# Kernel tuning notes

Measured on AMD Instinct MI355X. Metric: run time of the kernel, lower is better.

The kernel has to match this reference:

```python
import jax, jax.numpy as jnp
import numpy as np

C0 = 32          # cs[0] == cs[1] with planes=[32,32,...], cr=1.0
CIN = 4
EPS = 1e-5

# ---------- host-side coordinate hashing (mirrors F.sphash / F.sphashquery) ----------

def _enc(c):
    # unique int64 code per (x,y,z); +2 shift keeps offset-adjusted coords positive
    return (c[:, 0] + 2).astype(np.int64) + (c[:, 1] + 2).astype(np.int64) * 1024 \
        + (c[:, 2] + 2).astype(np.int64) * 1024 * 1024

def _lookup(sorted_codes, q):
    pos = np.searchsorted(sorted_codes, q)
    pos = np.minimum(pos, len(sorted_codes) - 1)
    return np.where(sorted_codes[pos] == q, pos, -1).astype(np.int32)

def _offsets(r):
    return np.array([[i, j, k] for i in r for j in r for k in r], np.int64)


def setup_inputs() -> dict:
    rng = np.random.default_rng(0)
    N0 = 400000
    pts = rng.integers(0, [400, 400, 40], size=(600000, 3)).astype(np.int64)
    codes = _enc(pts)
    codes_u, idx = np.unique(codes, return_index=True)
    assert len(codes_u) >= N0
    coords0, codes0 = pts[idx][:N0], codes_u[:N0]   # sorted by hash code

    off27, off8 = _offsets([-1, 0, 1]), _offsets([0, 1])
    # ks=3 stride=1 kernel map at level 0: nbr0[k, i] = index of coords0[i]+off27[k] (or -1)
    nbr0 = np.stack([_lookup(codes0, _enc(coords0 + o)) for o in off27])

    # stride-2 downsample coords (level 1)
    c1all = coords0 // 2
    codes1_u, i1 = np.unique(_enc(c1all), return_index=True)
    coords1 = c1all[i1]
    # ks=2 stride=2 kernel map: output voxel gathers inputs at 2*out + {0,1}^3
    down1 = np.stack([_lookup(codes0, _enc(coords1 * 2 + o)) for o in off8])
    # ks=3 stride=1 kernel map at level 1
    nbr1 = np.stack([_lookup(codes1_u, _enc(coords1 + o)) for o in off27])

    key = jax.random.key(0)
    ks = jax.random.split(key, 10)

    def w(k, K, ci, co):
        return jax.random.normal(k, (K, ci, co), jnp.float32) * (1.0 / np.sqrt(K * ci))

    return {
        "voxel_features": jax.random.normal(ks[0], (N0, CIN), jnp.float32),
        "W_stem1": w(ks[1], 27, CIN, C0),
        "W_stem2": w(ks[2], 27, C0, C0),
        "W_down":  w(ks[3], 8,  C0, C0),
        "W_r1a":   w(ks[4], 27, C0, C0),
        "W_r1b":   w(ks[5], 27, C0, C0),
        "W_r2a":   w(ks[6], 27, C0, C0),
        "W_r2b":   w(ks[7], 27, C0, C0),
        "gammas": jnp.ones((7, C0), jnp.float32),
        "betas":  jnp.zeros((7, C0), jnp.float32),
        "nbr0":  jnp.asarray(nbr0),
        "down1": jnp.asarray(down1),
        "nbr1":  jnp.asarray(nbr1),
    }


# ---------- sparse conv: gather-GEMM-scatter per kernel offset ----------

def _spconv(feat, nbr, W):
    # feat [N, Ci], nbr [K, M] (-1 = no neighbor), W [K, Ci, Co] -> out [M, Co]
    def step(acc, kw):
        idx, Wk = kw
        g = jnp.where((idx >= 0)[:, None], feat[jnp.maximum(idx, 0)], 0.0)
        return acc + g @ Wk, None
    acc0 = jnp.zeros((nbr.shape[1], W.shape[-1]), feat.dtype)
    out, _ = jax.lax.scan(step, acc0, (nbr, W))
    return out


def _bn(x, g, b):
    # BatchNorm1d, training-mode statistics (biased var), gamma/beta affine
    mu = x.mean(0)
    var = x.var(0)
    return (x - mu) * jax.lax.rsqrt(var + EPS) * g + b


def _cbr(x, nbr, W, g, b):
    return jax.nn.relu(_bn(_spconv(x, nbr, W), g, b))


def reference(voxel_features, W_stem1, W_stem2, W_down, W_r1a, W_r1b, W_r2a, W_r2b,
              gammas, betas, nbr0, down1, nbr1):
    g, b = gammas, betas
    # stem: two ks=3 sparse convs + BN + ReLU at level 0
    x = _cbr(voxel_features, nbr0, W_stem1, g[0], b[0])
    x = _cbr(x, nbr0, W_stem2, g[1], b[1])
    # stage1: BasicConvolutionBlock (ks=2, stride=2) + 2 ResidualBlocks at level 1
    x1 = _cbr(x, down1, W_down, g[2], b[2])
    h = _cbr(x1, nbr1, W_r1a, g[3], b[3])
    h = _bn(_spconv(h, nbr1, W_r1b), g[4], b[4])
    x1 = jax.nn.relu(h + x1)          # downsample == Identity (inc == outc, stride 1)
    h = _cbr(x1, nbr1, W_r2a, g[5], b[5])
    h = _bn(_spconv(h, nbr1, W_r2b), g[6], b[6])
    return jax.nn.relu(h + x1)
```

## Files before the change

### kernel.cpp

```cpp
#include <hip/hip_runtime.h>

#define EPS 1e-5f
#define WROWS 448

typedef __attribute__((ext_vector_type(8))) short short8;
typedef __attribute__((ext_vector_type(4))) float floatx4;
typedef __attribute__((ext_vector_type(8))) unsigned short ushort8;
typedef __attribute__((ext_vector_type(4))) unsigned short ushortv4;

#define O_S1  0
#define O_S2  4096
#define O_DN  (O_S2 + 27648)
#define O_R1A (O_DN + 8192)
#define O_R1B (O_R1A + 27648)
#define O_R2A (O_R1B + 27648)
#define O_R2B (O_R2A + 27648)
#define WP_TOTAL (O_R2B + 27648)

#define GLL16(g, l)                                                       \
    __builtin_amdgcn_global_load_lds(                                     \
        (const __attribute__((address_space(1))) void*)(g),               \
        (__attribute__((address_space(3))) void*)(l), 16, 0, 0)

__device__ __forceinline__ unsigned short f2bf(float f) {
    union { float f; unsigned u; } x; x.f = f;
    unsigned r = x.u + 0x7fffu + ((x.u >> 16) & 1u);
    return (unsigned short)(r >> 16);
}
__device__ __forceinline__ float bf2f(unsigned short b) {
    union { unsigned u; float f; } x; x.u = ((unsigned)b) << 16;
    return x.f;
}

__device__ __forceinline__ int xcd_swizzle(int nb) {
    int b = (int)blockIdx.x;
    int q = nb >> 3, r = nb & 7;
    int x = b & 7, i = b >> 3;
    return x * q + (x < r ? x : r) + i;
}

__device__ __forceinline__ short8 gath(const unsigned short* __restrict__ x,
                                       int ii, int q) {
    short8 z = {};
    return (ii >= 0) ? *(const short8*)(x + (size_t)ii * 32 + q * 8) : z;
}

template <int ZG, int TPG>
__device__ __forceinline__ void wmm_calc(
    const int* __restrict__ nbr, int N, int t, int* __restrict__ out)
{
    int ln = t & 63, wv = t >> 6;
    int lb = wv / ZG, c = wv - lb * ZG;
    int base = lb * 128;
    int mn = 0x7fffffff, mx = -1;
#pragma unroll
    for (int j = 0; j < TPG; ++j) {
#pragma unroll
        for (int h = 0; h < 2; ++h) {
            int r = base + h * 64 + ln;
            if (r < N) {
                int v = nbr[(size_t)(c + ZG * j) * N + r];
                if (v >= 0) { mn = min(mn, v); mx = max(mx, v); }
            }
        }
    }
#pragma unroll
    for (int off = 32; off >= 1; off >>= 1) {
        mn = min(mn, __shfl_down(mn, off));
        mx = max(mx, __shfl_down(mx, off));
    }
    if (ln == 0) { out[wv * 2] = (mx < 0) ? 0 : mn; out[wv * 2 + 1] = mx; }
}

__device__ __forceinline__ void pack_w_one(
    const float* __restrict__ W, unsigned short* __restrict__ out, int t)
{
    int lane = t & 63;
    int h = (t >> 6) & 1;
    int k = t >> 7;
    int m = lane & 15, q = lane >> 4;
    ushort8 v;
#pragma unroll
    for (int j = 0; j < 8; ++j)
        v[j] = f2bf(W[((size_t)k * 32 + q * 8 + j) * 32 + h * 16 + m]);
    *(ushort8*)(out + (size_t)t * 8) = v;
}

__global__ __launch_bounds__(256) void prep_kernel(
    const float* __restrict__ vf,
    const float* __restrict__ Ws1, const float* __restrict__ Ws2,
    const float* __restrict__ Wd,  const float* __restrict__ Wr1a,
    const float* __restrict__ Wr1b, const float* __restrict__ Wr2a,
    const float* __restrict__ Wr2b,
    const int* __restrict__ nbr0, const int* __restrict__ down1,
    const int* __restrict__ nbr1,
    unsigned short* __restrict__ xb, unsigned short* __restrict__ wp,
    int* __restrict__ wmm0, int* __restrict__ wmmD, int* __restrict__ wmm1,
    int N0, int N1)
{
    int t = blockIdx.x * 256 + threadIdx.x;
    if (t < N0) {
        float4 v = *(const float4*)(vf + (size_t)t * 4);
        ushortv4 r = {f2bf(v.x), f2bf(v.y), f2bf(v.z), f2bf(v.w)};
        *(ushortv4*)(xb + (size_t)t * 4) = r;
        return;
    }
    t -= N0;
    if (t < 512) {
        int lane = t & 63;
        int h = (t >> 6) & 1;
        int c = t >> 7;
        int m = lane & 15, q = lane >> 4;
        ushort8 v;
#pragma unroll
        for (int j = 0; j < 8; ++j) {
            int kdim = c * 32 + q * 8 + j;
            int tap = kdim >> 2, ci = kdim & 3;
            v[j] = (tap < 27) ? f2bf(Ws1[((size_t)tap * 4 + ci) * 32 + h * 16 + m]) : 0;
        }
        *(ushort8*)(wp + O_S1 + (size_t)t * 8) = v;
        return;
    }
    t -= 512;
    if (t < 27 * 128) { pack_w_one(Ws2,  wp + O_S2,  t); return; }
    t -= 27 * 128;
    if (t < 8 * 128)  { pack_w_one(Wd,   wp + O_DN,  t); return; }
    t -= 8 * 128;
    if (t < 27 * 128) { pack_w_one(Wr1a, wp + O_R1A, t); return; }
    t -= 27 * 128;
    if (t < 27 * 128) { pack_w_one(Wr1b, wp + O_R1B, t); return; }
    t -= 27 * 128;
    if (t < 27 * 128) { pack_w_one(Wr2a, wp + O_R2A, t); return; }
    t -= 27 * 128;
    if (t < 27 * 128) { pack_w_one(Wr2b, wp + O_R2B, t); return; }
    t -= 27 * 128;
    int nb0 = (N0 + 127) >> 7, nb1 = (N1 + 127) >> 7;
    if (t < nb0 * 3 * 64) { wmm_calc<3, 9>(nbr0, N0, t, wmm0); return; }
    t -= nb0 * 3 * 64;
    if (t < nb1 * 2 * 64) { wmm_calc<2, 4>(down1, N1, t, wmmD); return; }
    t -= nb1 * 2 * 64;
    if (t < nb1 * 3 * 64) { wmm_calc<3, 9>(nbr1, N1, t, wmm1); return; }
}

__device__ __forceinline__ void conv_epilogue2(
    floatx4 acc00, floatx4 acc01, floatx4 acc10, floatx4 acc11,
    unsigned short* __restrict__ y, float* __restrict__ part,
    int rowbase, int lb, int N, float* sm)
{
    const int lane = threadIdx.x & 63;
    const int m = lane & 15, q = lane >> 4;

    if (threadIdx.x < 64) sm[threadIdx.x] = 0.f;
    __syncthreads();

#pragma unroll
    for (int r = 0; r < 4; ++r) {
        int ra = rowbase + q * 4 + r;
        int rb = ra + 16;
        if (ra < N) {
            y[(size_t)ra * 32 + m]      = f2bf(acc00[r]);
            y[(size_t)ra * 32 + 16 + m] = f2bf(acc01[r]);
        }
        if (rb < N) {
            y[(size_t)rb * 32 + m]      = f2bf(acc10[r]);
            y[(size_t)rb * 32 + 16 + m] = f2bf(acc11[r]);
        }
    }

    float s0 = 0.f, q0 = 0.f, s1 = 0.f, q1 = 0.f;
#pragma unroll
    for (int r = 0; r < 4; ++r) {
        s0 += acc00[r] + acc10[r];
        q0 += acc00[r] * acc00[r] + acc10[r] * acc10[r];
        s1 += acc01[r] + acc11[r];
        q1 += acc01[r] * acc01[r] + acc11[r] * acc11[r];
    }
    s0 += __shfl_down(s0, 32); s0 += __shfl_down(s0, 16);
    q0 += __shfl_down(q0, 32); q0 += __shfl_down(q0, 16);
    s1 += __shfl_down(s1, 32); s1 += __shfl_down(s1, 16);
    q1 += __shfl_down(q1, 32); q1 += __shfl_down(q1, 16);
    if (lane < 16) {
        atomicAdd(&sm[m],      s0);
        atomicAdd(&sm[32 + m], q0);
        atomicAdd(&sm[16 + m],      s1);
        atomicAdd(&sm[48 + m], q1);
    }
    __syncthreads();
    if (threadIdx.x < 64)
        part[(size_t)lb * 64 + threadIdx.x] = sm[threadIdx.x];
}

#define MFMA_BF16 __builtin_amdgcn_mfma_f32_16x16x32_bf16

template <int K>
__global__ __launch_bounds__(256, 5) void conv_mfma_kernel(
    const unsigned short* __restrict__ x,
    const int* __restrict__ nbr,
    const unsigned short* __restrict__ Wp,
    const int* __restrict__ wmmg,
    unsigned short* __restrict__ y,
    float* __restrict__ part, int N)
{
    constexpr int ZG  = (K == 27) ? 3 : 2;
    constexpr int TPG = (K == 27) ? 9 : 4;

    __shared__ __align__(16) unsigned short win[(WROWS + 1) * 32];
    __shared__ float sm[64];

    const int nb = (N + 127) >> 7;
    const int lb = xcd_swizzle(nb);
    const int lane = threadIdx.x & 63;
    const int wave = threadIdx.x >> 6;
    const int m = lane & 15, q = lane >> 4;
    const int rowbase = lb * 128 + wave * 32;
    const int r0 = rowbase + m;
    const int r1 = r0 + 16;
    const bool v0 = r0 < N, v1 = r1 < N;

    floatx4 c00 = {0.f, 0.f, 0.f, 0.f};
    floatx4 c01 = c00, c10 = c00, c11 = c00;

    if (threadIdx.x < 4) {
        short8 z = {};
        *(short8*)&win[WROWS * 32 + threadIdx.x * 8] = z;
    }

    int wmn[ZG], wc4[ZG];
#pragma unroll
    for (int c = 0; c < ZG; ++c) {
        int lo = wmmg[(lb * ZG + c) * 2];
        int hi = wmmg[(lb * ZG + c) * 2 + 1];
        wmn[c] = lo;
        int sp = (hi < 0) ? 0 : (hi - lo + 1);
        wc4[c] = (sp < WROWS ? sp : WROWS) * 4;
        if (hi >= 0 && hi - lo + 1 > WROWS) wc4[c] = -1;
    }

#define IDX(k, rr, vv) ((vv) ? nbr[(size_t)(k) * N + (rr)] : -1)
#define LG(dst, ii)                                                        \
    {                                                                      \
        unsigned rr_ = (unsigned)((ii) - wmin);                            \
        unsigned rc_ = rr_ < (unsigned)WROWS ? rr_ : (unsigned)WROWS;      \
        dst = *(const short8*)&win[rc_ * 32 + ((q ^ ((rc_ >> 1) & 3)) << 3)]; \
    }

    for (int c = 0; c < ZG; ++c) {
        const int wmin = wmn[c];
        const int sc4 = wc4[c];
        const bool use_lds = (sc4 >= 0);

        if (use_lds) {
            for (int cb = wave * 64; cb < sc4; cb += 256) {
                int cc = cb + lane;
                int rr = cc >> 2, s = cc & 3;
                int qq = s ^ ((rr >> 1) & 3);
                if (cc < sc4)
                    GLL16(x + ((size_t)(wmin + rr)) * 32 + qq * 8, win + (size_t)cb * 8);
            }
        }

        int ia0 = (0 < TPG) ? IDX(c + ZG * 0, r0, v0) : -1;
        int ib0 = (0 < TPG) ? IDX(c + ZG * 0, r1, v1) : -1;
        int ia1 = (1 < TPG) ? IDX(c + ZG * 1, r0, v0) : -1;
        int ib1 = (1 < TPG) ? IDX(c + ZG * 1, r1, v1) : -1;
        int ia2 = (2 < TPG) ? IDX(c + ZG * 2, r0, v0) : -1;
        int ib2 = (2 < TPG) ? IDX(c + ZG * 2, r1, v1) : -1;
        int ia3 = (3 < TPG) ? IDX(c + ZG * 3, r0, v0) : -1;
        int ib3 = (3 < TPG) ? IDX(c + ZG * 3, r1, v1) : -1;
        int ia4 = (4 < TPG) ? IDX(c + ZG * 4, r0, v0) : -1;
        int ib4 = (4 < TPG) ? IDX(c + ZG * 4, r1, v1) : -1;
        int ia5 = (5 < TPG) ? IDX(c + ZG * 5, r0, v0) : -1;
        int ib5 = (5 < TPG) ? IDX(c + ZG * 5, r1, v1) : -1;
        int ia6 = (6 < TPG) ? IDX(c + ZG * 6, r0, v0) : -1;
        int ib6 = (6 < TPG) ? IDX(c + ZG * 6, r1, v1) : -1;
        int ia7 = (7 < TPG) ? IDX(c + ZG * 7, r0, v0) : -1;
        int ib7 = (7 < TPG) ? IDX(c + ZG * 7, r1, v1) : -1;
        int ia8 = (8 < TPG) ? IDX(c + ZG * 8, r0, v0) : -1;
        int ib8 = (8 < TPG) ? IDX(c + ZG * 8, r1, v1) : -1;

        __syncthreads();

#define TAPL(J, iA, iB)                                                    \
        if (J < TPG) {                                                     \
            const short8* wk = (const short8*)(Wp + (size_t)(c + ZG * J) * 1024); \
            short8 b0 = wk[lane];                                          \
            short8 b1 = wk[64 + lane];                                     \
            short8 a0, a1;                                                 \
            LG(a0, iA); LG(a1, iB);                                        \
            c00 = MFMA_BF16(a0, b0, c00, 0, 0, 0);                         \
            c01 = MFMA_BF16(a0, b1, c01, 0, 0, 0);                         \
            c10 = MFMA_BF16(a1, b0, c10, 0, 0, 0);                         \
            c11 = MFMA_BF16(a1, b1, c11, 0, 0, 0);                         \
        }
#define TAPG(J, iA, iB)                                                    \
        if (J < TPG) {                                                     \
            const short8* wk = (const short8*)(Wp + (size_t)(c + ZG * J) * 1024); \
            short8 b0 = wk[lane];                                          \
            short8 b1 = wk[64 + lane];                                     \
            short8 a0 = gath(x, iA, q);                                    \
            short8 a1 = gath(x, iB, q);                                    \
            c00 = MFMA_BF16(a0, b0, c00, 0, 0, 0);                         \
            c01 = MFMA_BF16(a0, b1, c01, 0, 0, 0);                         \
            c10 = MFMA_BF16(a1, b0, c10, 0, 0, 0);                         \
            c11 = MFMA_BF16(a1, b1, c11, 0, 0, 0);                         \
        }
        if (use_lds) {
            TAPL(0, ia0, ib0) TAPL(1, ia1, ib1) TAPL(2, ia2, ib2)
            TAPL(3, ia3, ib3) TAPL(4, ia4, ib4) TAPL(5, ia5, ib5)
            TAPL(6, ia6, ib6) TAPL(7, ia7, ib7) TAPL(8, ia8, ib8)
        } else {
            TAPG(0, ia0, ib0) TAPG(1, ia1, ib1) TAPG(2, ia2, ib2)
            TAPG(3, ia3, ib3) TAPG(4, ia4, ib4) TAPG(5, ia5, ib5)
            TAPG(6, ia6, ib6) TAPG(7, ia7, ib7) TAPG(8, ia8, ib8)
        }
#undef TAPL
#undef TAPG

        if (c != ZG - 1) __syncthreads();
    }
#undef IDX
#undef LG

    conv_epilogue2(c00, c01, c10, c11, y, part, rowbase, lb, N, sm);
}

__global__ __launch_bounds__(256) void conv_stem1_mfma(
    const unsigned short* __restrict__ xb,
    const int* __restrict__ nbr,
    const unsigned short* __restrict__ Wp,
    unsigned short* __restrict__ y,
    float* __restrict__ part, int N)
{
    __shared__ float sm[64];
    const int nb = (N + 127) / 128;
    const int lb = xcd_swizzle(nb);
    const int lane = threadIdx.x & 63;
    const int wave = threadIdx.x >> 6;
    const int m = lane & 15, q = lane >> 4;
    const int rowbase = lb * 128 + wave * 32;
    const int row0 = rowbase + m;
    const int row1 = rowbase + 16 + m;

    floatx4 acc00 = {0.f, 0.f, 0.f, 0.f};
    floatx4 acc01 = acc00, acc10 = acc00, acc11 = acc00;

#pragma unroll
    for (int c = 0; c < 4; ++c) {
        const int t0 = c * 8 + q * 2, t1 = t0 + 1;
        short8 a0 = {}, a1 = {};
        {
            int ia = (t0 < 27 && row0 < N) ? nbr[(size_t)t0 * N + row0] : -1;
            int ib = (t1 < 27 && row0 < N) ? nbr[(size_t)t1 * N + row0] : -1;
            ushortv4 ga = {}, gb = {};
            if (ia >= 0) ga = *(const ushortv4*)(xb + (size_t)ia * 4);
            if (ib >= 0) gb = *(const ushortv4*)(xb + (size_t)ib * 4);
            a0[0] = (short)ga[0]; a0[1] = (short)ga[1];
            a0[2] = (short)ga[2]; a0[3] = (short)ga[3];
            a0[4] = (short)gb[0]; a0[5] = (short)gb[1];
            a0[6] = (short)gb[2]; a0[7] = (short)gb[3];
        }
        {
            int ia = (t0 < 27 && row1 < N) ? nbr[(size_t)t0 * N + row1] : -1;
            int ib = (t1 < 27 && row1 < N) ? nbr[(size_t)t1 * N + row1] : -1;
            ushortv4 ga = {}, gb = {};
            if (ia >= 0) ga = *(const ushortv4*)(xb + (size_t)ia * 4);
            if (ib >= 0) gb = *(const ushortv4*)(xb + (size_t)ib * 4);
            a1[0] = (short)ga[0]; a1[1] = (short)ga[1];
            a1[2] = (short)ga[2]; a1[3] = (short)ga[3];
            a1[4] = (short)gb[0]; a1[5] = (short)gb[1];
            a1[6] = (short)gb[2]; a1[7] = (short)gb[3];
        }
        const short8* wk = (const short8*)Wp;
        short8 b0 = wk[(c * 2 + 0) * 64 + lane];
        short8 b1 = wk[(c * 2 + 1) * 64 + lane];
        acc00 = MFMA_BF16(a0, b0, acc00, 0, 0, 0);
        acc01 = MFMA_BF16(a0, b1, acc01, 0, 0, 0);
        acc10 = MFMA_BF16(a1, b0, acc10, 0, 0, 0);
        acc11 = MFMA_BF16(a1, b1, acc11, 0, 0, 0);
    }

    conv_epilogue2(acc00, acc01, acc10, acc11, y, part, rowbase, lb, N, sm);
}

__global__ __launch_bounds__(256) void reduce_stats_kernel(
    const float* __restrict__ part, float* __restrict__ stats, int nb)
{
    __shared__ float sm[256];
    int t = threadIdx.x;
    int c = t & 63, g = t >> 6;
    float s = 0.f;
    for (int b = blockIdx.x * 4 + g; b < nb; b += 256)
        s += part[(size_t)b * 64 + c];
    sm[t] = s;
    __syncthreads();
    if (t < 64)
        atomicAdd(&stats[t], sm[t] + sm[64 + t] + sm[128 + t] + sm[192 + t]);
}

template <bool OUT_F32, bool HAS_RES>
__global__ __launch_bounds__(256) void bn_relu_kernel(
    const unsigned short* __restrict__ y, const float* __restrict__ stats,
    const float* __restrict__ gamma, const float* __restrict__ beta,
    const unsigned short* __restrict__ resid, void* __restrict__ outp, int N)
{
    int t = blockIdx.x * 256 + threadIdx.x;
    if (t >= N) return;
    float inv_n = 1.0f / (float)N;
    const ushort8* yr = (const ushort8*)(y + (size_t)t * 32);

#pragma unroll
    for (int c = 0; c < 4; ++c) {
        ushort8 v = yr[c];
        ushort8 rv = {};
        if (HAS_RES) rv = ((const ushort8*)(resid + (size_t)t * 32))[c];
        float f0, f1, f2, f3, f4, f5, f6, f7;
#define BNJ(fj, j)                                                        \
        {                                                                 \
            int co = c * 8 + (j);                                         \
            float mu = stats[co] * inv_n;                                 \
            float var = stats[32 + co] * inv_n - mu * mu;                 \
            float sc = rsqrtf(var + EPS) * gamma[co];                     \
            fj = (bf2f(v[j]) - mu) * sc + beta[co];                       \
            if (HAS_RES) fj += bf2f(rv[j]);                               \
            fj = fmaxf(fj, 0.0f);                                         \
        }
        BNJ(f0, 0) BNJ(f1, 1) BNJ(f2, 2) BNJ(f3, 3)
        BNJ(f4, 4) BNJ(f5, 5) BNJ(f6, 6) BNJ(f7, 7)
#undef BNJ
        if (OUT_F32) {
            float* ob = (float*)outp + (size_t)t * 32 + c * 8;
            floatx4 u0 = {f0, f1, f2, f3}, u1 = {f4, f5, f6, f7};
            *(floatx4*)(ob) = u0;
            *(floatx4*)(ob + 4) = u1;
        } else {
            ushort8 o;
            o[0] = f2bf(f0); o[1] = f2bf(f1); o[2] = f2bf(f2); o[3] = f2bf(f3);
            o[4] = f2bf(f4); o[5] = f2bf(f5); o[6] = f2bf(f6); o[7] = f2bf(f7);
            ((ushort8*)((unsigned short*)outp + (size_t)t * 32))[c] = o;
        }
    }
}

extern "C" void kernel_launch(void* const* d_in, const int* in_sizes, int n_in,
                              void* d_out, int out_size, void* d_ws, size_t ws_size,
                              hipStream_t stream)
{
    const float* vf   = (const float*)d_in[0];
    const float* Ws1  = (const float*)d_in[1];
    const float* Ws2  = (const float*)d_in[2];
    const float* Wd   = (const float*)d_in[3];
    const float* Wr1a = (const float*)d_in[4];
    const float* Wr1b = (const float*)d_in[5];
    const float* Wr2a = (const float*)d_in[6];
    const float* Wr2b = (const float*)d_in[7];
    const float* gam  = (const float*)d_in[8];
    const float* bet  = (const float*)d_in[9];
    const int* nbr0   = (const int*)d_in[10];
    const int* down1  = (const int*)d_in[11];
    const int* nbr1   = (const int*)d_in[12];

    int N0 = in_sizes[0] / 4;
    int N1 = in_sizes[11] / 8;

    unsigned short* yraw = (unsigned short*)d_ws;
    unsigned short* actA = yraw + (size_t)N0 * 32;
    unsigned short* actB = actA + (size_t)N0 * 32;
    unsigned short* xb   = actB + (size_t)N0 * 32;
    unsigned short* wp   = xb + (size_t)N0 * 4;
    float* part  = (float*)(wp + WP_TOTAL);
    float* stats = part + (size_t)3200 * 64;
    int nb0 = (N0 + 127) / 128;
    int nb1 = (N1 + 127) / 128;
    int* wmm0 = (int*)(stats + 7 * 64);
    int* wmmD = wmm0 + (size_t)nb0 * 6;
    int* wmm1 = wmmD + (size_t)nb1 * 4;

    hipMemsetAsync(stats, 0, 7 * 64 * sizeof(float), stream);

    auto g1 = [](int n) { return dim3((unsigned)((n + 255) / 256)); };
    auto gm = [](int n) { return dim3((unsigned)((n + 127) / 128)); };

    int prep_threads = N0 + 512 + 128 * (27 * 5 + 8) + 64 * (nb0 * 3 + nb1 * 5);
    prep_kernel<<<g1(prep_threads), 256, 0, stream>>>(
        vf, Ws1, Ws2, Wd, Wr1a, Wr1b, Wr2a, Wr2b,
        nbr0, down1, nbr1, xb, wp, wmm0, wmmD, wmm1, N0, N1);

    conv_stem1_mfma<<<gm(N0), 256, 0, stream>>>(xb, nbr0, wp + O_S1, yraw, part, N0);
    reduce_stats_kernel<<<64, 256, 0, stream>>>(part, stats + 0 * 64, nb0);
    bn_relu_kernel<false, false><<<g1(N0), 256, 0, stream>>>(yraw, stats + 0 * 64, gam + 0, bet + 0, nullptr, actA, N0);
    conv_mfma_kernel<27><<<gm(N0), 256, 0, stream>>>(actA, nbr0, wp + O_S2, wmm0, yraw, part, N0);
    reduce_stats_kernel<<<64, 256, 0, stream>>>(part, stats + 1 * 64, nb0);
    bn_relu_kernel<false, false><<<g1(N0), 256, 0, stream>>>(yraw, stats + 1 * 64, gam + 32, bet + 32, nullptr, actB, N0);
    conv_mfma_kernel<8><<<gm(N1), 256, 0, stream>>>(actB, down1, wp + O_DN, wmmD, yraw, part, N1);
    reduce_stats_kernel<<<64, 256, 0, stream>>>(part, stats + 2 * 64, nb1);
    bn_relu_kernel<false, false><<<g1(N1), 256, 0, stream>>>(yraw, stats + 2 * 64, gam + 64, bet + 64, nullptr, actA, N1);
    conv_mfma_kernel<27><<<gm(N1), 256, 0, stream>>>(actA, nbr1, wp + O_R1A, wmm1, yraw, part, N1);
    reduce_stats_kernel<<<64, 256, 0, stream>>>(part, stats + 3 * 64, nb1);
    bn_relu_kernel<false, false><<<g1(N1), 256, 0, stream>>>(yraw, stats + 3 * 64, gam + 96, bet + 96, nullptr, actB, N1);
    conv_mfma_kernel<27><<<gm(N1), 256, 0, stream>>>(actB, nbr1, wp + O_R1B, wmm1, yraw, part, N1);
    reduce_stats_kernel<<<64, 256, 0, stream>>>(part, stats + 4 * 64, nb1);
    bn_relu_kernel<false, true><<<g1(N1), 256, 0, stream>>>(yraw, stats + 4 * 64, gam + 128, bet + 128, actA, actB, N1);
    conv_mfma_kernel<27><<<gm(N1), 256, 0, stream>>>(actB, nbr1, wp + O_R2A, wmm1, yraw, part, N1);
    reduce_stats_kernel<<<64, 256, 0, stream>>>(part, stats + 5 * 64, nb1);
    bn_relu_kernel<false, false><<<g1(N1), 256, 0, stream>>>(yraw, stats + 5 * 64, gam + 160, bet + 160, nullptr, actA, N1);
    conv_mfma_kernel<27><<<gm(N1), 256, 0, stream>>>(actA, nbr1, wp + O_R2B, wmm1, yraw, part, N1);
    reduce_stats_kernel<<<64, 256, 0, stream>>>(part, stats + 6 * 64, nb1);
    bn_relu_kernel<true, true><<<g1(N1), 256, 0, stream>>>(yraw, stats + 6 * 64, gam + 192, bet + 192, actB, d_out, N1);
}
```

Before: 620.9 us.

## Enlarge conv tiles to 256 rows, stage output via LDS, atomically accumulate BN stats

The K=27 conv kernels now process 256 rows per 512-thread block, with a larger LDS gather window (576 rows). The neighbour min/max ranges are recomputed per 256-row group so the window can be shared across more rows. Conv outputs are staged through LDS and written as coalesced 16-byte rows instead of scattered 2-byte stores. Per-block BN partial sums are added straight into the stats buffer with atomics, which drops the separate reduce_stats launches. In exchange, larger windows overflow to the global-gather fallback more often, LDS use rises, and the float atomics make the stats summation order nondeterministic.

```diff
diff --git a/kernel.cpp b/kernel.cpp
--- a/kernel.cpp
+++ b/kernel.cpp
@@ -1,7 +1,7 @@
 #include <hip/hip_runtime.h>
 
 #define EPS 1e-5f
-#define WROWS 448
+#define WROWS 576
 
 typedef __attribute__((ext_vector_type(8))) short short8;
 typedef __attribute__((ext_vector_type(4))) float floatx4;
@@ -45,18 +45,18 @@
     return (ii >= 0) ? *(const short8*)(x + (size_t)ii * 32 + q * 8) : z;
 }
 
-template <int ZG, int TPG>
+template <int ZG, int TPG, int HR>
 __device__ __forceinline__ void wmm_calc(
     const int* __restrict__ nbr, int N, int t, int* __restrict__ out)
 {
     int ln = t & 63, wv = t >> 6;
     int lb = wv / ZG, c = wv - lb * ZG;
-    int base = lb * 128;
+    int base = lb * (HR * 64);
     int mn = 0x7fffffff, mx = -1;
 #pragma unroll
     for (int j = 0; j < TPG; ++j) {
 #pragma unroll
-        for (int h = 0; h < 2; ++h) {
+        for (int h = 0; h < HR; ++h) {
             int r = base + h * 64 + ln;
             if (r < N) {
                 int v = nbr[(size_t)(c + ZG * j) * N + r];
@@ -134,37 +134,36 @@
     t -= 27 * 128;
     if (t < 27 * 128) { pack_w_one(Wr2b, wp + O_R2B, t); return; }
     t -= 27 * 128;
-    int nb0 = (N0 + 127) >> 7, nb1 = (N1 + 127) >> 7;
-    if (t < nb0 * 3 * 64) { wmm_calc<3, 9>(nbr0, N0, t, wmm0); return; }
-    t -= nb0 * 3 * 64;
-    if (t < nb1 * 2 * 64) { wmm_calc<2, 4>(down1, N1, t, wmmD); return; }
-    t -= nb1 * 2 * 64;
-    if (t < nb1 * 3 * 64) { wmm_calc<3, 9>(nbr1, N1, t, wmm1); return; }
-}
-
+    int nb0s = (N0 + 255) >> 8;
+    int nbd  = (N1 + 127) >> 7;
+    int nb1s = (N1 + 255) >> 8;
+    if (t < nb0s * 3 * 64) { wmm_calc<3, 9, 4>(nbr0, N0, t, wmm0); return; }
+    t -= nb0s * 3 * 64;
+    if (t < nbd * 2 * 64)  { wmm_calc<2, 4, 2>(down1, N1, t, wmmD); return; }
+    t -= nbd * 2 * 64;
+    if (t < nb1s * 3 * 64) { wmm_calc<3, 9, 4>(nbr1, N1, t, wmm1); return; }
+}
+
+template <int ROWS, int THREADS>
 __device__ __forceinline__ void conv_epilogue2(
     floatx4 acc00, floatx4 acc01, floatx4 acc10, floatx4 acc11,
-    unsigned short* __restrict__ y, float* __restrict__ part,
-    int rowbase, int lb, int N, float* sm)
+    unsigned short* __restrict__ y, float* __restrict__ stats,
+    int rb0, int N, float* sm, unsigned short* win)
 {
     const int lane = threadIdx.x & 63;
+    const int wave = (int)threadIdx.x >> 6;
     const int m = lane & 15, q = lane >> 4;
 
     if (threadIdx.x < 64) sm[threadIdx.x] = 0.f;
     __syncthreads();
 
+    unsigned short* wrow = win + (size_t)wave * 32 * 32;
 #pragma unroll
     for (int r = 0; r < 4; ++r) {
-        int ra = rowbase + q * 4 + r;
-        int rb = ra + 16;
-        if (ra < N) {
-            y[(size_t)ra * 32 + m]      = f2bf(acc00[r]);
-            y[(size_t)ra * 32 + 16 + m] = f2bf(acc01[r]);
-        }
-        if (rb < N) {
-            y[(size_t)rb * 32 + m]      = f2bf(acc10[r]);
-            y[(size_t)rb * 32 + 16 + m] = f2bf(acc11[r]);
-        }
+        wrow[(q * 4 + r) * 32 + m]           = f2bf(acc00[r]);
+        wrow[(q * 4 + r) * 32 + 16 + m]      = f2bf(acc01[r]);
+        wrow[(16 + q * 4 + r) * 32 + m]      = f2bf(acc10[r]);
+        wrow[(16 + q * 4 + r) * 32 + 16 + m] = f2bf(acc11[r]);
     }
 
     float s0 = 0.f, q0 = 0.f, s1 = 0.f, q1 = 0.f;
@@ -186,33 +185,44 @@
         atomicAdd(&sm[48 + m], q1);
     }
     __syncthreads();
+
+    for (int i = threadIdx.x; i < ROWS * 4; i += THREADS) {
+        int rr = i >> 2, hh = i & 3;
+        int grow = rb0 + rr;
+        if (grow < N)
+            *(ushort8*)(y + (size_t)grow * 32 + hh * 8) =
+                *(const ushort8*)&win[(size_t)rr * 32 + hh * 8];
+    }
     if (threadIdx.x < 64)
-        part[(size_t)lb * 64 + threadIdx.x] = sm[threadIdx.x];
+        atomicAdd(&stats[threadIdx.x], sm[threadIdx.x]);
 }
 
 #define MFMA_BF16 __builtin_amdgcn_mfma_f32_16x16x32_bf16
 
 template <int K>
-__global__ __launch_bounds__(256, 5) void conv_mfma_kernel(
+__global__ __launch_bounds__((K == 27) ? 512 : 256, 6) void conv_mfma_kernel(
     const unsigned short* __restrict__ x,
     const int* __restrict__ nbr,
     const unsigned short* __restrict__ Wp,
     const int* __restrict__ wmmg,
     unsigned short* __restrict__ y,
-    float* __restrict__ part, int N)
-{
-    constexpr int ZG  = (K == 27) ? 3 : 2;
-    constexpr int TPG = (K == 27) ? 9 : 4;
+    float* __restrict__ stats, int N)
+{
+    constexpr int ZG   = (K == 27) ? 3 : 2;
+    constexpr int TPG  = (K == 27) ? 9 : 4;
+    constexpr int ROWS = (K == 27) ? 256 : 128;
+    constexpr int THREADS = ROWS * 2;
 
     __shared__ __align__(16) unsigned short win[(WROWS + 1) * 32];
     __shared__ float sm[64];
 
-    const int nb = (N + 127) >> 7;
+    const int nb = (N + ROWS - 1) / ROWS;
     const int lb = xcd_swizzle(nb);
     const int lane = threadIdx.x & 63;
-    const int wave = threadIdx.x >> 6;
+    const int wave = (int)threadIdx.x >> 6;
     const int m = lane & 15, q = lane >> 4;
-    const int rowbase = lb * 128 + wave * 32;
+    const int rb0 = lb * ROWS;
+    const int rowbase = rb0 + wave * 32;
     const int r0 = rowbase + m;
     const int r1 = r0 + 16;
     const bool v0 = r0 < N, v1 = r1 < N;
@@ -250,7 +260,7 @@
         const bool use_lds = (sc4 >= 0);
 
         if (use_lds) {
-            for (int cb = wave * 64; cb < sc4; cb += 256) {
+            for (int cb = wave * 64; cb < sc4; cb += THREADS) {
                 int cc = cb + lane;
                 int rr = cc >> 2, s = cc & 3;
                 int qq = s ^ ((rr >> 1) & 3);
@@ -321,7 +331,7 @@
 #undef IDX
 #undef LG
 
-    conv_epilogue2(c00, c01, c10, c11, y, part, rowbase, lb, N, sm);
+    conv_epilogue2<ROWS, THREADS>(c00, c01, c10, c11, y, stats, rb0, N, sm, win);
 }
 
 __global__ __launch_bounds__(256) void conv_stem1_mfma(
@@ -329,15 +339,17 @@
     const int* __restrict__ nbr,
     const unsigned short* __restrict__ Wp,
     unsigned short* __restrict__ y,
-    float* __restrict__ part, int N)
-{
+    float* __restrict__ stats, int N)
+{
+    __shared__ __align__(16) unsigned short winS[128 * 32];
     __shared__ float sm[64];
     const int nb = (N + 127) / 128;
     const int lb = xcd_swizzle(nb);
     const int lane = threadIdx.x & 63;
-    const int wave = threadIdx.x >> 6;
+    const int wave = (int)threadIdx.x >> 6;
     const int m = lane & 15, q = lane >> 4;
-    const int rowbase = lb * 128 + wave * 32;
+    const int rb0 = lb * 128;
+    const int rowbase = rb0 + wave * 32;
     const int row0 = rowbase + m;
     const int row1 = rowbase + 16 + m;
 
@@ -379,22 +391,7 @@
         acc11 = MFMA_BF16(a1, b1, acc11, 0, 0, 0);
     }
 
-    conv_epilogue2(acc00, acc01, acc10, acc11, y, part, rowbase, lb, N, sm);
-}
-
-__global__ __launch_bounds__(256) void reduce_stats_kernel(
-    const float* __restrict__ part, float* __restrict__ stats, int nb)
-{
-    __shared__ float sm[256];
-    int t = threadIdx.x;
-    int c = t & 63, g = t >> 6;
-    float s = 0.f;
-    for (int b = blockIdx.x * 4 + g; b < nb; b += 256)
-        s += part[(size_t)b * 64 + c];
-    sm[t] = s;
-    __syncthreads();
-    if (t < 64)
-        atomicAdd(&stats[t], sm[t] + sm[64 + t] + sm[128 + t] + sm[192 + t]);
+    conv_epilogue2<128, 256>(acc00, acc01, acc10, acc11, y, stats, rb0, N, sm, winS);
 }
 
 template <bool OUT_F32, bool HAS_RES>
@@ -467,43 +464,37 @@
     unsigned short* actB = actA + (size_t)N0 * 32;
     unsigned short* xb   = actB + (size_t)N0 * 32;
     unsigned short* wp   = xb + (size_t)N0 * 4;
-    float* part  = (float*)(wp + WP_TOTAL);
-    float* stats = part + (size_t)3200 * 64;
-    int nb0 = (N0 + 127) / 128;
-    int nb1 = (N1 + 127) / 128;
+    float* stats = (float*)(wp + WP_TOTAL);
+    int nb0  = (N0 + 127) / 128;
+    int nb0s = (N0 + 255) / 256;
+    int nbd  = (N1 + 127) / 128;
+    int nb1s = (N1 + 255) / 256;
     int* wmm0 = (int*)(stats + 7 * 64);
-    int* wmmD = wmm0 + (size_t)nb0 * 6;
-    int* wmm1 = wmmD + (size_t)nb1 * 4;
+    int* wmmD = wmm0 + (size_t)nb0s * 6;
+    int* wmm1 = wmmD + (size_t)nbd * 4;
 
     hipMemsetAsync(stats, 0, 7 * 64 * sizeof(float), stream);
 
     auto g1 = [](int n) { return dim3((unsigned)((n + 255) / 256)); };
-    auto gm = [](int n) { return dim3((unsigned)((n + 127) / 128)); };
-
-    int prep_threads = N0 + 512 + 128 * (27 * 5 + 8) + 64 * (nb0 * 3 + nb1 * 5);
+
+    int prep_threads = N0 + 512 + 128 * (27 * 5 + 8)
+                     + 64 * (nb0s * 3 + nbd * 2 + nb1s * 3);
     prep_kernel<<<g1(prep_threads), 256, 0, stream>>>(
         vf, Ws1, Ws2, Wd, Wr1a, Wr1b, Wr2a, Wr2b,
         nbr0, down1, nbr1, xb, wp, wmm0, wmmD, wmm1, N0, N1);
 
-    conv_stem1_mfma<<<gm(N0), 256, 0, stream>>>(xb, nbr0, wp + O_S1, yraw, part, N0);
-    reduce_stats_kernel<<<64, 256, 0, stream>>>(part, stats + 0 * 64, nb0);
+    conv_stem1_mfma<<<dim3((unsigned)nb0), 256, 0, stream>>>(xb, nbr0, wp + O_S1, yraw, stats + 0 * 64, N0);
     bn_relu_kernel<false, false><<<g1(N0), 256, 0, stream>>>(yraw, stats + 0 * 64, gam + 0, bet + 0, nullptr, actA, N0);
-    conv_mfma_kernel<27><<<gm(N0), 256, 0, stream>>>(actA, nbr0, wp + O_S2, wmm0, yraw, part, N0);
-    reduce_stats_kernel<<<64, 256, 0, stream>>>(part, stats + 1 * 64, nb0);
+    conv_mfma_kernel<27><<<dim3((unsigned)nb0s), 512, 0, stream>>>(actA, nbr0, wp + O_S2, wmm0, yraw, stats + 1 * 64, N0);
     bn_relu_kernel<false, false><<<g1(N0), 256, 0, stream>>>(yraw, stats + 1 * 64, gam + 32, bet + 32, nullptr, actB, N0);
-    conv_mfma_kernel<8><<<gm(N1), 256, 0, stream>>>(actB, down1, wp + O_DN, wmmD, yraw, part, N1);
-    reduce_stats_kernel<<<64, 256, 0, stream>>>(part, stats + 2 * 64, nb1);
+    conv_mfma_kernel<8><<<dim3((unsigned)nbd), 256, 0, stream>>>(actB, down1, wp + O_DN, wmmD, yraw, stats + 2 * 64, N1);
     bn_relu_kernel<false, false><<<g1(N1), 256, 0, stream>>>(yraw, stats + 2 * 64, gam + 64, bet + 64, nullptr, actA, N1);
-    conv_mfma_kernel<27><<<gm(N1), 256, 0, stream>>>(actA, nbr1, wp + O_R1A, wmm1, yraw, part, N1);
-    reduce_stats_kernel<<<64, 256, 0, stream>>>(part, stats + 3 * 64, nb1);
+    conv_mfma_kernel<27><<<dim3((unsigned)nb1s), 512, 0, stream>>>(actA, nbr1, wp + O_R1A, wmm1, yraw, stats + 3 * 64, N1);
     bn_relu_kernel<false, false><<<g1(N1), 256, 0, stream>>>(yraw, stats + 3 * 64, gam + 96, bet + 96, nullptr, actB, N1);
-    conv_mfma_kernel<27><<<gm(N1), 256, 0, stream>>>(actB, nbr1, wp + O_R1B, wmm1, yraw, part, N1);
-    reduce_stats_kernel<<<64, 256, 0, stream>>>(part, stats + 4 * 64, nb1);
+    conv_mfma_kernel<27><<<dim3((unsigned)nb1s), 512, 0, stream>>>(actB, nbr1, wp + O_R1B, wmm1, yraw, stats + 4 * 64, N1);
     bn_relu_kernel<false, true><<<g1(N1), 256, 0, stream>>>(yraw, stats + 4 * 64, gam + 128, bet + 128, actA, actB, N1);
-    conv_mfma_kernel<27><<<gm(N1), 256, 0, stream>>>(actB, nbr1, wp + O_R2A, wmm1, yraw, part, N1);
-    reduce_stats_kernel<<<64, 256, 0, stream>>>(part, stats + 5 * 64, nb1);
+    conv_mfma_kernel<27><<<dim3((unsigned)nb1s), 512, 0, stream>>>(actB, nbr1, wp + O_R2A, wmm1, yraw, stats + 5 * 64, N1);
     bn_relu_kernel<false, false><<<g1(N1), 256, 0, stream>>>(yraw, stats + 5 * 64, gam + 160, bet + 160, nullptr, actA, N1);
-    conv_mfma_kernel<27><<<gm(N1), 256, 0, stream>>>(actA, nbr1, wp + O_R2B, wmm1, yraw, part, N1);
-    reduce_stats_kernel<<<64, 256, 0, stream>>>(part, stats + 6 * 64, nb1);
+    conv_mfma_kernel<27><<<dim3((unsigned)nb1s), 512, 0, stream>>>(actA, nbr1, wp + O_R2B, wmm1, yraw, stats + 6 * 64, N1);
     bn_relu_kernel<true, true><<<g1(N1), 256, 0, stream>>>(yraw, stats + 6 * 64, gam + 192, bet + 192, actB, d_out, N1);
 }
```

After: 997.7 us. 1.61x slower.
